# Kernel optimization log

Measured on AMD Instinct MI355X. Metric: run time of the kernel, lower is better.

## Reference

```python
import jax, jax.numpy as jnp
import numpy as np

EPS = 1e-5
N_HEADS = 16
D_NOPE = 128
D_ROPE = 64
D_QK = D_NOPE + D_ROPE  # 192
D_V = 128
KV_RANK = 512
SCALE = D_QK ** -0.5


def rms_norm(x, w, eps=EPS):
    return x * jax.lax.rsqrt(jnp.mean(x * x, axis=-1, keepdims=True) + eps) * w


def apply_rope(x, c, s):
    # x: [..., D_ROPE], c/s broadcastable [..., D_ROPE//2]; half-split rotation
    x0, x1 = x[..., : D_ROPE // 2], x[..., D_ROPE // 2 :]
    return jnp.concatenate([x0 * c - x1 * s, x0 * s + x1 * c], axis=-1)


def setup_inputs() -> dict:
    key = jax.random.key(0)
    ks = jax.random.split(key, 8)
    B, S, H_DIM = 2, 2048, 2048
    Q_RANK = 1536
    w = lambda k, shp: jax.random.normal(k, shp, dtype=jnp.float32) * 0.02
    # real RoPE tables: [max_seq, D_ROPE//2]
    inv_freq = 1.0 / (10000.0 ** (np.arange(0, D_ROPE, 2, dtype=np.float32) / D_ROPE))
    ang = np.arange(S, dtype=np.float32)[:, None] * inv_freq[None, :]
    return {
        "x": jax.random.normal(ks[0], (B, S, H_DIM), dtype=jnp.float32),
        "positions": jnp.arange(S, dtype=jnp.int64),
        "Wqa": w(ks[1], (H_DIM, Q_RANK)),
        "g_qa": jnp.ones((Q_RANK,), jnp.float32),
        "Wqb": w(ks[2], (Q_RANK, N_HEADS * D_QK)),
        "Wkva": w(ks[3], (H_DIM, KV_RANK + D_ROPE)),
        "g_kva": jnp.ones((KV_RANK,), jnp.float32),
        "Wkvb": w(ks[4], (KV_RANK, N_HEADS * (D_NOPE + D_V))),
        "Wo": w(ks[5], (N_HEADS * D_V, H_DIM)),
        "cos": jnp.asarray(np.cos(ang)),
        "sin": jnp.asarray(np.sin(ang)),
    }


def reference(x, positions, Wqa, g_qa, Wqb, Wkva, g_kva, Wkvb, Wo, cos, sin):
    B, S, _ = x.shape
    # Q path: low-rank down, RMSNorm, up
    q = rms_norm(x @ Wqa, g_qa) @ Wqb  # [B,S,H*D_QK]
    q = q.reshape(B, S, N_HEADS, D_QK)
    q_nope, q_rope = q[..., :D_NOPE], q[..., D_NOPE:]
    c = cos[positions]  # [S, D_ROPE//2]
    s = sin[positions]
    q_rope = apply_rope(q_rope, c[None, :, None, :], s[None, :, None, :])
    # KV path: joint down-proj, split latent / rope-key
    kv_a = x @ Wkva  # [B,S,KV_RANK+D_ROPE]
    kv_latent = rms_norm(kv_a[..., :KV_RANK], g_kva)
    k_rope = apply_rope(kv_a[..., KV_RANK:], c[None, :, :], s[None, :, :])  # [B,S,D_ROPE]
    # up-project latent to per-head k_nope and v
    kv_b = (kv_latent @ Wkvb).reshape(B, S, N_HEADS, D_NOPE + D_V)
    k_nope, v = kv_b[..., :D_NOPE], kv_b[..., D_NOPE:]
    k = jnp.concatenate(
        [k_nope, jnp.broadcast_to(k_rope[:, :, None, :], (B, S, N_HEADS, D_ROPE))], axis=-1
    )  # [B,S,H,D_QK]
    q_full = jnp.concatenate([q_nope, q_rope], axis=-1)  # [B,S,H,D_QK]
    # causal SDPA with d_qk != d_v
    scores = jnp.einsum("bqhd,bkhd->bhqk", q_full, k) * SCALE
    causal = jnp.tril(jnp.ones((S, S), dtype=bool))
    scores = jnp.where(causal[None, None, :, :], scores, -jnp.inf)
    p = jax.nn.softmax(scores, axis=-1)
    out = jnp.einsum("bhqk,bkhd->bqhd", p, v).reshape(B, S, N_HEADS * D_V)
    return out @ Wo
```

## Files before the change

kernel.cpp:

```cpp
#include <hip/hip_runtime.h>
#include <hip/hip_bf16.h>

typedef __bf16 bf16;
typedef __bf16 bf16x8 __attribute__((ext_vector_type(8)));
typedef __bf16 bf16x4 __attribute__((ext_vector_type(4)));
typedef float f32x4 __attribute__((ext_vector_type(4)));

#define B_    2
#define S_    2048
#define HD    2048
#define NH    16
#define DQK   192
#define DV    128
#define QR    1536
#define KVR   512
#define NTOK  4096
#define NKVB  4096
#define NQB   3072
#define NQKVA 2176

#define EXP2F(x) __builtin_amdgcn_exp2f(x)

static __device__ __forceinline__ void gload16(const void* g, void* l) {
  __builtin_amdgcn_global_load_lds(
      (const __attribute__((address_space(1))) void*)g,
      (__attribute__((address_space(3))) void*)l, 16, 0, 0);
}

__global__ __launch_bounds__(256) void cvt_bf16(const float* __restrict__ in,
                                                bf16* __restrict__ out, long n) {
  long i = ((long)blockIdx.x * 256 + threadIdx.x) * 4;
  if (i + 3 < n) {
    float4 v = *(const float4*)(in + i);
    bf16x4 o = {(bf16)v.x, (bf16)v.y, (bf16)v.z, (bf16)v.w};
    *(bf16x4*)(out + i) = o;
  }
}

struct TransArgs {
  const float *s0, *s1, *s2, *s3, *s4;
  bf16 *d0, *d1, *d2, *d3, *d4;
};
__global__ __launch_bounds__(256) void transpose_all(TransArgs a) {
  __shared__ float tile[32][33];
  int bid = blockIdx.x;
  int seg, rel;
  if      (bid < 3072)  { seg = 0; rel = bid; }
  else if (bid < 4352)  { seg = 1; rel = bid - 3072; }
  else if (bid < 8960)  { seg = 2; rel = bid - 4352; }
  else if (bid < 11008) { seg = 3; rel = bid - 8960; }
  else                  { seg = 4; rel = bid - 11008; }
  const float* in = seg == 0 ? a.s0 : seg == 1 ? a.s1 : seg == 2 ? a.s2 : seg == 3 ? a.s3 : a.s4;
  bf16* out       = seg == 0 ? a.d0 : seg == 1 ? a.d1 : seg == 2 ? a.d2 : seg == 3 ? a.d3 : a.d4;
  int R   = seg == 0 ? 2048 : seg == 1 ? 2048 : seg == 2 ? 1536 : seg == 3 ? 512 : 2048;
  int C   = seg == 0 ? 1536 : seg == 1 ? 576  : seg == 2 ? 3072 : seg == 3 ? 4096 : 2048;
  int Np  = seg == 0 ? 1536 : seg == 1 ? 640  : seg == 2 ? 3072 : seg == 3 ? 4096 : 2048;
  int nbx = seg == 0 ? 48   : seg == 1 ? 20   : seg == 2 ? 96   : seg == 3 ? 128 : 64;
  int c0 = (rel % nbx) * 32;
  int r0 = (rel / nbx) * 32;
  int tx = threadIdx.x & 31, ty = threadIdx.x >> 5;
#pragma unroll
  for (int i = 0; i < 4; ++i) {
    int r = r0 + ty + i * 8, c = c0 + tx;
    tile[ty + i * 8][tx] = (c < C) ? in[(long)r * C + c] : 0.f;
  }
  __syncthreads();
#pragma unroll
  for (int i = 0; i < 4; ++i) {
    int oc = c0 + ty + i * 8;
    if (oc < Np) out[(long)oc * R + r0 + tx] = (bf16)tile[tx][ty + i * 8];
  }
}

#define GEMM_CORE(A, Bt, K)                                                    \
  __shared__ bf16 As[128 * 64];                                                \
  __shared__ bf16 Bs[128 * 64];                                                \
  const int t = threadIdx.x;                                                   \
  const int l = t & 63;                                                        \
  const int w = t >> 6;                                                        \
  const int m0 = blockIdx.y * 128;                                             \
  const int n0 = blockIdx.x * 128;                                             \
  const int wr = (w >> 1) * 64;                                                \
  const int wc = (w & 1) * 64;                                                 \
  const int lr = l & 15;                                                       \
  const int lg = l >> 4;                                                       \
  f32x4 acc[4][4] = {};                                                        \
  for (int k0 = 0; k0 < (K); k0 += 64) {                                       \
    __syncthreads();                                                           \
    _Pragma("unroll")                                                          \
    for (int j = 0; j < 4; ++j) {                                              \
      int s = j * 256 + t;                                                     \
      int row = s >> 3, sc = s & 7;                                            \
      int c = sc ^ (row & 7);                                                  \
      gload16((A) + (long)(m0 + row) * (K) + k0 + c * 8,                       \
              As + (j * 256 + w * 64) * 8);                                    \
      gload16((Bt) + (long)(n0 + row) * (K) + k0 + c * 8,                      \
              Bs + (j * 256 + w * 64) * 8);                                    \
    }                                                                          \
    __syncthreads();                                                           \
    _Pragma("unroll")                                                          \
    for (int kh = 0; kh < 2; ++kh) {                                           \
      bf16x8 af[4], bfr[4];                                                    \
      _Pragma("unroll")                                                        \
      for (int m = 0; m < 4; ++m) {                                            \
        int row = wr + m * 16 + lr;                                            \
        af[m] = *(const bf16x8*)(As + row * 64 + (((kh * 4 + lg) ^ (row & 7)) << 3)); \
      }                                                                        \
      _Pragma("unroll")                                                        \
      for (int n = 0; n < 4; ++n) {                                            \
        int row = wc + n * 16 + lr;                                            \
        bfr[n] = *(const bf16x8*)(Bs + row * 64 + (((kh * 4 + lg) ^ (row & 7)) << 3)); \
      }                                                                        \
      _Pragma("unroll")                                                        \
      for (int m = 0; m < 4; ++m)                                              \
        _Pragma("unroll")                                                      \
        for (int n = 0; n < 4; ++n)                                            \
          acc[m][n] = __builtin_amdgcn_mfma_f32_16x16x32_bf16(af[m], bfr[n], acc[m][n], 0, 0, 0); \
    }                                                                          \
  }

template <typename CT>
__global__ __launch_bounds__(256) void gemm_bf16(const bf16* __restrict__ A,
                                                 const bf16* __restrict__ Bt,
                                                 CT* __restrict__ C,
                                                 int M, int N, int K) {
  GEMM_CORE(A, Bt, K)
#pragma unroll
  for (int m = 0; m < 4; ++m)
#pragma unroll
    for (int n = 0; n < 4; ++n)
#pragma unroll
      for (int v = 0; v < 4; ++v) {
        int row = m0 + wr + m * 16 + lg * 4 + v;
        int col = n0 + wc + n * 16 + lr;
        C[(long)row * N + col] = (CT)acc[m][n][v];
      }
}

__global__ __launch_bounds__(256) void gemm_qf(const bf16* __restrict__ A,
                                               const bf16* __restrict__ Bt,
                                               const int* __restrict__ pos,
                                               const float* __restrict__ cosT,
                                               const float* __restrict__ sinT,
                                               bf16* __restrict__ q_bhsd) {
  const float SCALE = 0.07216878364870323f * 1.4426950408889634f;
  GEMM_CORE(A, Bt, QR)
  int c0 = n0 + wc;
  int h = c0 / 192;
  int part = c0 - h * 192;
#pragma unroll
  for (int m = 0; m < 4; ++m)
#pragma unroll
    for (int v = 0; v < 4; ++v) {
      int row = m0 + wr + m * 16 + lg * 4 + v;
      int b = row >> 11, s = row & (S_ - 1);
      long base = ((long)(b * NH + h) * S_ + s) * DQK;
      if (part < 128) {
#pragma unroll
        for (int n = 0; n < 4; ++n)
          q_bhsd[base + part + n * 16 + lr] = (bf16)(acc[m][n][v] * SCALE);
      } else {
        int p = pos[s] & (S_ - 1);
        float c_lo = cosT[p * 32 + lr],      s_lo = sinT[p * 32 + lr];
        float c_hi = cosT[p * 32 + 16 + lr], s_hi = sinT[p * 32 + 16 + lr];
        float o0 = acc[m][0][v] * c_lo - acc[m][2][v] * s_lo;
        float o1 = acc[m][1][v] * c_hi - acc[m][3][v] * s_hi;
        float o2 = acc[m][0][v] * s_lo + acc[m][2][v] * c_lo;
        float o3 = acc[m][1][v] * s_hi + acc[m][3][v] * c_hi;
        q_bhsd[base + 128 + lr] = (bf16)(o0 * SCALE);
        q_bhsd[base + 144 + lr] = (bf16)(o1 * SCALE);
        q_bhsd[base + 160 + lr] = (bf16)(o2 * SCALE);
        q_bhsd[base + 176 + lr] = (bf16)(o3 * SCALE);
      }
    }
}

__global__ __launch_bounds__(256) void gemm_kvb(const bf16* __restrict__ A,
                                                const bf16* __restrict__ Bt,
                                                bf16* __restrict__ k_bhsd,
                                                bf16* __restrict__ v_rows) {
  GEMM_CORE(A, Bt, KVR)
  int c0 = n0 + wc;
  int h = c0 >> 8;
  int dbase = c0 & 64;
  bool vpart = (c0 >> 7) & 1;
#pragma unroll
  for (int m = 0; m < 4; ++m)
#pragma unroll
    for (int v = 0; v < 4; ++v) {
      int row = m0 + wr + m * 16 + lg * 4 + v;
      int b = row >> 11, s = row & (S_ - 1);
      if (!vpart) {
        long base = ((long)(b * NH + h) * S_ + s) * DQK + dbase;
#pragma unroll
        for (int n = 0; n < 4; ++n)
          k_bhsd[base + n * 16 + lr] = (bf16)acc[m][n][v];
      } else {
        long base = (long)row * 2048 + h * 128 + dbase;
#pragma unroll
        for (int n = 0; n < 4; ++n)
          v_rows[base + n * 16 + lr] = (bf16)acc[m][n][v];
      }
    }
}

__global__ __launch_bounds__(256) void norm_prep(const bf16* __restrict__ xa,
                                                 const float* __restrict__ g_qa,
                                                 const float* __restrict__ g_kva,
                                                 const int* __restrict__ pos,
                                                 const float* __restrict__ cosT,
                                                 const float* __restrict__ sinT,
                                                 bf16* __restrict__ q_n,
                                                 bf16* __restrict__ kv_l,
                                                 bf16* __restrict__ k_bhsd) {
  int row = blockIdx.x;
  int t = threadIdx.x;
  int b = row >> 11, s = row & (S_ - 1);
  const bf16* xr = xa + (long)row * NQKVA;
  __shared__ float red[3];
  __shared__ bf16 rope_s[64];
  float vf[8];
  if (t < 192) {
    bf16x8 vv = *(const bf16x8*)(xr + t * 8);
    float ss = 0.f;
#pragma unroll
    for (int e = 0; e < 8; ++e) { vf[e] = (float)vv[e]; ss += vf[e] * vf[e]; }
#pragma unroll
    for (int m = 1; m < 64; m <<= 1) ss += __shfl_xor(ss, m);
    if ((t & 63) == 0) red[t >> 6] = ss;
  } else {
    int tt = t - 192;
    const bf16* xl = xr + QR;
    bf16x8 vv = *(const bf16x8*)(xl + tt * 8);
    float ss = 0.f;
#pragma unroll
    for (int e = 0; e < 8; ++e) { vf[e] = (float)vv[e]; ss += vf[e] * vf[e]; }
#pragma unroll
    for (int m = 1; m < 64; m <<= 1) ss += __shfl_xor(ss, m);
    float rs = rsqrtf(ss / KVR + 1e-5f);
    bf16x8 o;
#pragma unroll
    for (int e = 0; e < 8; ++e) o[e] = (bf16)(vf[e] * rs * g_kva[tt * 8 + e]);
    *(bf16x8*)(kv_l + (long)row * KVR + tt * 8) = o;
    if (tt < 32) {
      int p = pos[s] & (S_ - 1);
      float c = cosT[p * 32 + tt], sn = sinT[p * 32 + tt];
      float x0 = (float)xl[512 + tt], x1 = (float)xl[544 + tt];
      rope_s[tt] = (bf16)(x0 * c - x1 * sn);
      rope_s[32 + tt] = (bf16)(x0 * sn + x1 * c);
    }
  }
  __syncthreads();
  if (t < 192) {
    float ss = red[0] + red[1] + red[2];
    float rs = rsqrtf(ss / QR + 1e-5f);
    bf16x8 o;
#pragma unroll
    for (int e = 0; e < 8; ++e) o[e] = (bf16)(vf[e] * rs * g_qa[t * 8 + e]);
    *(bf16x8*)(q_n + (long)row * QR + t * 8) = o;
  } else {
    int tt = t - 192;
    bf16x8 rv = *(const bf16x8*)&rope_s[(tt & 7) * 8];
    long base0 = ((long)(b * NH + (tt >> 3)) * S_ + s) * DQK + 128 + (tt & 7) * 8;
    long base1 = ((long)(b * NH + 8 + (tt >> 3)) * S_ + s) * DQK + 128 + (tt & 7) * 8;
    *(bf16x8*)(k_bhsd + base0) = rv;
    *(bf16x8*)(k_bhsd + base1) = rv;
  }
}

__global__ __launch_bounds__(256) void v_trans(const bf16* __restrict__ v_rows,
                                               bf16* __restrict__ v_t) {
  __shared__ bf16 tile[32][33];
  int st = blockIdx.x, dt = blockIdx.y, bh = blockIdx.z;
  int b = bh >> 4, h = bh & 15;
  int tx = threadIdx.x & 31, ty = threadIdx.x >> 5;
#pragma unroll
  for (int i = 0; i < 4; ++i) {
    int s = st * 32 + ty + i * 8, d = dt * 32 + tx;
    tile[ty + i * 8][tx] = v_rows[((long)(b * S_ + s)) * 2048 + h * 128 + d];
  }
  __syncthreads();
#pragma unroll
  for (int i = 0; i < 4; ++i) {
    int d = dt * 32 + ty + i * 8, s = st * 32 + tx;
    v_t[((long)bh * DV + d) * S_ + s] = tile[tx][ty + i * 8];
  }
}

#define QBLK 64
#define KVB  64
#define DVP  144
__global__ __launch_bounds__(256) void flash2(const bf16* __restrict__ q_bhsd,
                                              const bf16* __restrict__ k_bhsd,
                                              const bf16* __restrict__ v_t,
                                              bf16* __restrict__ att) {
  __shared__ bf16 Ks[KVB * DQK];
  __shared__ bf16 Vs[DVP * KVB];
  __shared__ bf16 Ps[4][16 * 72];
  int bid = blockIdx.x;
  int bh = bid & 31;
  int qt = 31 - (bid >> 5);
  int b = bh >> 4, h = bh & 15;
  int q0 = qt * QBLK;
  int t = threadIdx.x;
  int w = t >> 6, l = t & 63;
  int lr = l & 15, lg = l >> 4;
  int qw = q0 + w * 16;

  const bf16* Qb = q_bhsd + (long)bh * S_ * DQK;
  const bf16* Kb = k_bhsd + (long)bh * S_ * DQK;
  const bf16* Vb = v_t + (long)bh * DV * S_;

  if (t < 128) {
    int rr = 128 + (t >> 3), cc = (t & 7) * 8;
    bf16 val = (bf16)((rr == 128) ? 1.0f : 0.0f);
    bf16x8 vvv = {val, val, val, val, val, val, val, val};
    *(bf16x8*)(Vs + rr * KVB + cc) = vvv;
  }

  bf16x8 qf[6];
#pragma unroll
  for (int t6 = 0; t6 < 6; ++t6)
    qf[t6] = *(const bf16x8*)(Qb + (long)(qw + lr) * DQK + t6 * 32 + lg * 8);

  f32x4 oacc[9] = {};
  float mrow[4] = {-1e30f, -1e30f, -1e30f, -1e30f};
  const int lr7 = lr & 7;

  int nkt = qt + 1;
  for (int kt = 0; kt < nkt; ++kt) {
    int k0 = kt * KVB;
    __syncthreads();
#pragma unroll
    for (int j = 0; j < 6; ++j) {
      int s = j * 256 + t;
      int r = s / 24, c1 = s - r * 24;
      int c = c1 ^ (r & 7);
      gload16(Kb + (long)(k0 + r) * DQK + c * 8, Ks + (j * 256 + w * 64) * 8);
    }
#pragma unroll
    for (int j = 0; j < 4; ++j) {
      int s = j * 256 + t;
      int d = s >> 3, c1 = s & 7;
      int c = c1 ^ (d & 7);
      gload16(Vb + (long)d * S_ + k0 + c * 8, Vs + (j * 256 + w * 64) * 8);
    }
    __syncthreads();
    if (k0 > qw + 15) continue;

    f32x4 sacc[4] = {};
#pragma unroll
    for (int n = 0; n < 4; ++n) {
      int rk = n * 16 + lr;
#pragma unroll
      for (int t6 = 0; t6 < 6; ++t6) {
        bf16x8 kf = *(const bf16x8*)(Ks + rk * DQK + (((t6 * 4 + lg) ^ lr7) << 3));
        sacc[n] = __builtin_amdgcn_mfma_f32_16x16x32_bf16(qf[t6], kf, sacc[n], 0, 0, 0);
      }
    }
    if (k0 + KVB - 1 > qw) {
#pragma unroll
      for (int n = 0; n < 4; ++n)
#pragma unroll
        for (int v = 0; v < 4; ++v) {
          int r = lg * 4 + v, c = n * 16 + lr;
          if (k0 + c > qw + r) sacc[n][v] = -1e30f;
        }
    }
    float mv[4];
#pragma unroll
    for (int v = 0; v < 4; ++v) {
      mv[v] = fmaxf(fmaxf(sacc[0][v], sacc[1][v]), fmaxf(sacc[2][v], sacc[3][v]));
#pragma unroll
      for (int msk = 1; msk < 16; msk <<= 1) mv[v] = fmaxf(mv[v], __shfl_xor(mv[v], msk));
    }
    bool grow = (mv[0] > mrow[0] + 8.f) | (mv[1] > mrow[1] + 8.f) |
                (mv[2] > mrow[2] + 8.f) | (mv[3] > mrow[3] + 8.f);
    if (__any(grow)) {
      float corr[4];
#pragma unroll
      for (int v = 0; v < 4; ++v) {
        float mt = fmaxf(mrow[v], mv[v]);
        corr[v] = EXP2F(mrow[v] - mt);
        mrow[v] = mt;
      }
#pragma unroll
      for (int dn = 0; dn < 9; ++dn)
#pragma unroll
        for (int v = 0; v < 4; ++v) oacc[dn][v] *= corr[v];
    }
#pragma unroll
    for (int v = 0; v < 4; ++v)
#pragma unroll
      for (int n = 0; n < 4; ++n)
        Ps[w][(lg * 4 + v) * 72 + n * 16 + lr] = (bf16)EXP2F(sacc[n][v] - mrow[v]);
#pragma unroll
    for (int kc = 0; kc < 2; ++kc) {
      bf16x8 pf = *(const bf16x8*)(Ps[w] + lr * 72 + kc * 32 + lg * 8);
#pragma unroll
      for (int dn = 0; dn < 9; ++dn) {
        int d = dn * 16 + lr;
        bf16x8 vf = *(const bf16x8*)(Vs + d * KVB + (((kc * 4 + lg) ^ lr7) << 3));
        oacc[dn] = __builtin_amdgcn_mfma_f32_16x16x32_bf16(pf, vf, oacc[dn], 0, 0, 0);
      }
    }
  }
  float rl[4];
#pragma unroll
  for (int v = 0; v < 4; ++v) {
    float lv = __shfl(oacc[8][v], lg * 16);
    rl[v] = 1.0f / lv;
  }
#pragma unroll
  for (int dn = 0; dn < 8; ++dn)
#pragma unroll
    for (int v = 0; v < 4; ++v) {
      int r = lg * 4 + v;
      float o = oacc[dn][v] * rl[v];
      att[((long)(b * S_ + qw + r)) * 2048 + h * 128 + dn * 16 + lr] = (bf16)o;
    }
}

extern "C" void kernel_launch(void* const* d_in, const int* in_sizes, int n_in,
                              void* d_out, int out_size, void* d_ws, size_t ws_size,
                              hipStream_t stream) {
  const float* x        = (const float*)d_in[0];
  const int* pos        = (const int*)d_in[1];
  const float* Wqa      = (const float*)d_in[2];
  const float* g_qa     = (const float*)d_in[3];
  const float* Wqb      = (const float*)d_in[4];
  const float* Wkva     = (const float*)d_in[5];
  const float* g_kva    = (const float*)d_in[6];
  const float* Wkvb     = (const float*)d_in[7];
  const float* Wo       = (const float*)d_in[8];
  const float* cosT     = (const float*)d_in[9];
  const float* sinT     = (const float*)d_in[10];
  float* out            = (float*)d_out;

  size_t off = 0;
  char* wsp = (char*)d_ws;
  auto alloc = [&](size_t n) { void* p = wsp + off; off += (n + 255) & ~(size_t)255; return p; };
  bf16*  Wqa_t  = (bf16*) alloc((size_t)QR * HD * 2);
  bf16*  Wkva_t = (bf16*) alloc((size_t)640 * HD * 2);
  bf16*  Wqb_t  = (bf16*) alloc((size_t)NQB * QR * 2);
  bf16*  Wkvb_t = (bf16*) alloc((size_t)NKVB * KVR * 2);
  bf16*  Wo_t   = (bf16*) alloc((size_t)HD * HD * 2);
  bf16*  x_bf   = (bf16*) alloc((size_t)NTOK * HD * 2);
  bf16*  q_bhsd = (bf16*) alloc((size_t)B_ * NH * S_ * DQK * 2);
  bf16*  k_bhsd = (bf16*) alloc((size_t)B_ * NH * S_ * DQK * 2);
  bf16*  v_rows = (bf16*) alloc((size_t)NTOK * 2048 * 2);
  bf16*  v_t    = (bf16*) alloc((size_t)B_ * NH * DV * S_ * 2);
  bf16*  att    = (bf16*) alloc((size_t)NTOK * 2048 * 2);
  char*  T      = (char*) alloc((size_t)33554432);
  bf16*  xa  = (bf16*)T;
  bf16*  q_n = (bf16*)(T + 18874368);
  bf16*  kv_l = (bf16*)(T + 18874368 + 12582912);
  if (ws_size < off) return;

  cvt_bf16<<<(NTOK * HD / 4 + 255) / 256, 256, 0, stream>>>(x, x_bf, (long)NTOK * HD);
  TransArgs ta = {Wqa, Wkva, Wqb, Wkvb, Wo, Wqa_t, Wkva_t, Wqb_t, Wkvb_t, Wo_t};
  transpose_all<<<15104, 256, 0, stream>>>(ta);
  gemm_bf16<bf16><<<dim3(NQKVA / 128, NTOK / 128), 256, 0, stream>>>(x_bf, Wqa_t, xa, NTOK, NQKVA, HD);
  norm_prep<<<NTOK, 256, 0, stream>>>(xa, g_qa, g_kva, pos, cosT, sinT, q_n, kv_l, k_bhsd);
  gemm_qf<<<dim3(NQB / 128, NTOK / 128), 256, 0, stream>>>(q_n, Wqb_t, pos, cosT, sinT, q_bhsd);
  gemm_kvb<<<dim3(NKVB / 128, NTOK / 128), 256, 0, stream>>>(kv_l, Wkvb_t, k_bhsd, v_rows);
  v_trans<<<dim3(S_ / 32, DV / 32, B_ * NH), 256, 0, stream>>>(v_rows, v_t);
  flash2<<<1024, 256, 0, stream>>>(q_bhsd, k_bhsd, v_t, att);
  gemm_bf16<float><<<dim3(HD / 128, NTOK / 128), 256, 0, stream>>>(att, Wo_t, out, NTOK, HD, HD);
}
```

Baseline: 325.3 us.

## Fuse V transpose into KV-up GEMM epilogue and enlarge flash query tile

The KV up-projection epilogue now writes V directly in transposed [b,h,d,s] layout as 4-wide bf16 stores, so the separate v_trans kernel and the v_rows buffer are removed. The attention kernel is widened to 512 threads (8 waves) with 128-query tiles, which halves the number of blocks and shares each K/V tile load across twice as many query rows. The trade-offs are narrower strided stores in the GEMM epilogue, more causal-tail imbalance per block, and higher shared-memory and register pressure per block.

```diff
diff --git a/kernel.cpp b/kernel.cpp
--- a/kernel.cpp
+++ b/kernel.cpp
@@ -178,30 +178,38 @@
 __global__ __launch_bounds__(256) void gemm_kvb(const bf16* __restrict__ A,
                                                 const bf16* __restrict__ Bt,
                                                 bf16* __restrict__ k_bhsd,
-                                                bf16* __restrict__ v_rows) {
+                                                bf16* __restrict__ v_t) {
   GEMM_CORE(A, Bt, KVR)
   int c0 = n0 + wc;
   int h = c0 >> 8;
   int dbase = c0 & 64;
   bool vpart = (c0 >> 7) & 1;
-#pragma unroll
-  for (int m = 0; m < 4; ++m)
-#pragma unroll
-    for (int v = 0; v < 4; ++v) {
-      int row = m0 + wr + m * 16 + lg * 4 + v;
-      int b = row >> 11, s = row & (S_ - 1);
-      if (!vpart) {
+  if (!vpart) {
+#pragma unroll
+    for (int m = 0; m < 4; ++m)
+#pragma unroll
+      for (int v = 0; v < 4; ++v) {
+        int row = m0 + wr + m * 16 + lg * 4 + v;
+        int b = row >> 11, s = row & (S_ - 1);
         long base = ((long)(b * NH + h) * S_ + s) * DQK + dbase;
 #pragma unroll
         for (int n = 0; n < 4; ++n)
           k_bhsd[base + n * 16 + lr] = (bf16)acc[m][n][v];
-      } else {
-        long base = (long)row * 2048 + h * 128 + dbase;
-#pragma unroll
-        for (int n = 0; n < 4; ++n)
-          v_rows[base + n * 16 + lr] = (bf16)acc[m][n][v];
-      }
-    }
+      }
+  } else {
+#pragma unroll
+    for (int m = 0; m < 4; ++m) {
+      int row0 = m0 + wr + m * 16 + lg * 4;
+      int b = row0 >> 11, s = row0 & (S_ - 1);
+#pragma unroll
+      for (int n = 0; n < 4; ++n) {
+        int d = dbase + n * 16 + lr;
+        bf16x4 o = {(bf16)acc[m][n][0], (bf16)acc[m][n][1],
+                    (bf16)acc[m][n][2], (bf16)acc[m][n][3]};
+        *(bf16x4*)(v_t + ((long)(b * NH + h) * DV + d) * S_ + s) = o;
+      }
+    }
+  }
 }
 
 __global__ __launch_bounds__(256) void norm_prep(const bf16* __restrict__ xa,
@@ -268,40 +276,20 @@
   }
 }
 
-__global__ __launch_bounds__(256) void v_trans(const bf16* __restrict__ v_rows,
-                                               bf16* __restrict__ v_t) {
-  __shared__ bf16 tile[32][33];
-  int st = blockIdx.x, dt = blockIdx.y, bh = blockIdx.z;
-  int b = bh >> 4, h = bh & 15;
-  int tx = threadIdx.x & 31, ty = threadIdx.x >> 5;
-#pragma unroll
-  for (int i = 0; i < 4; ++i) {
-    int s = st * 32 + ty + i * 8, d = dt * 32 + tx;
-    tile[ty + i * 8][tx] = v_rows[((long)(b * S_ + s)) * 2048 + h * 128 + d];
-  }
-  __syncthreads();
-#pragma unroll
-  for (int i = 0; i < 4; ++i) {
-    int d = dt * 32 + ty + i * 8, s = st * 32 + tx;
-    v_t[((long)bh * DV + d) * S_ + s] = tile[tx][ty + i * 8];
-  }
-}
-
-#define QBLK 64
 #define KVB  64
 #define DVP  144
-__global__ __launch_bounds__(256) void flash2(const bf16* __restrict__ q_bhsd,
+__global__ __launch_bounds__(512) void flash4(const bf16* __restrict__ q_bhsd,
                                               const bf16* __restrict__ k_bhsd,
                                               const bf16* __restrict__ v_t,
                                               bf16* __restrict__ att) {
   __shared__ bf16 Ks[KVB * DQK];
   __shared__ bf16 Vs[DVP * KVB];
-  __shared__ bf16 Ps[4][16 * 72];
+  __shared__ bf16 Ps[8][16 * 72];
   int bid = blockIdx.x;
   int bh = bid & 31;
-  int qt = 31 - (bid >> 5);
+  int qt = 15 - (bid >> 5);
   int b = bh >> 4, h = bh & 15;
-  int q0 = qt * QBLK;
+  int q0 = qt * 128;
   int t = threadIdx.x;
   int w = t >> 6, l = t & 63;
   int lr = l & 15, lg = l >> 4;
@@ -327,23 +315,23 @@
   float mrow[4] = {-1e30f, -1e30f, -1e30f, -1e30f};
   const int lr7 = lr & 7;
 
-  int nkt = qt + 1;
+  int nkt = 2 * qt + 2;
   for (int kt = 0; kt < nkt; ++kt) {
     int k0 = kt * KVB;
     __syncthreads();
 #pragma unroll
-    for (int j = 0; j < 6; ++j) {
-      int s = j * 256 + t;
+    for (int j = 0; j < 3; ++j) {
+      int s = j * 512 + t;
       int r = s / 24, c1 = s - r * 24;
       int c = c1 ^ (r & 7);
-      gload16(Kb + (long)(k0 + r) * DQK + c * 8, Ks + (j * 256 + w * 64) * 8);
-    }
-#pragma unroll
-    for (int j = 0; j < 4; ++j) {
-      int s = j * 256 + t;
+      gload16(Kb + (long)(k0 + r) * DQK + c * 8, Ks + (j * 512 + w * 64) * 8);
+    }
+#pragma unroll
+    for (int j = 0; j < 2; ++j) {
+      int s = j * 512 + t;
       int d = s >> 3, c1 = s & 7;
       int c = c1 ^ (d & 7);
-      gload16(Vb + (long)d * S_ + k0 + c * 8, Vs + (j * 256 + w * 64) * 8);
+      gload16(Vb + (long)d * S_ + k0 + c * 8, Vs + (j * 512 + w * 64) * 8);
     }
     __syncthreads();
     if (k0 > qw + 15) continue;
@@ -448,7 +436,6 @@
   bf16*  x_bf   = (bf16*) alloc((size_t)NTOK * HD * 2);
   bf16*  q_bhsd = (bf16*) alloc((size_t)B_ * NH * S_ * DQK * 2);
   bf16*  k_bhsd = (bf16*) alloc((size_t)B_ * NH * S_ * DQK * 2);
-  bf16*  v_rows = (bf16*) alloc((size_t)NTOK * 2048 * 2);
   bf16*  v_t    = (bf16*) alloc((size_t)B_ * NH * DV * S_ * 2);
   bf16*  att    = (bf16*) alloc((size_t)NTOK * 2048 * 2);
   char*  T      = (char*) alloc((size_t)33554432);
@@ -463,8 +450,7 @@
   gemm_bf16<bf16><<<dim3(NQKVA / 128, NTOK / 128), 256, 0, stream>>>(x_bf, Wqa_t, xa, NTOK, NQKVA, HD);
   norm_prep<<<NTOK, 256, 0, stream>>>(xa, g_qa, g_kva, pos, cosT, sinT, q_n, kv_l, k_bhsd);
   gemm_qf<<<dim3(NQB / 128, NTOK / 128), 256, 0, stream>>>(q_n, Wqb_t, pos, cosT, sinT, q_bhsd);
-  gemm_kvb<<<dim3(NKVB / 128, NTOK / 128), 256, 0, stream>>>(kv_l, Wkvb_t, k_bhsd, v_rows);
-  v_trans<<<dim3(S_ / 32, DV / 32, B_ * NH), 256, 0, stream>>>(v_rows, v_t);
-  flash2<<<1024, 256, 0, stream>>>(q_bhsd, k_bhsd, v_t, att);
+  gemm_kvb<<<dim3(NKVB / 128, NTOK / 128), 256, 0, stream>>>(kv_l, Wkvb_t, k_bhsd, v_t);
+  flash4<<<512, 512, 0, stream>>>(q_bhsd, k_bhsd, v_t, att);
   gemm_bf16<float><<<dim3(HD / 128, NTOK / 128), 256, 0, stream>>>(att, Wo_t, out, NTOK, HD, HD);
 }
```

Measured after the change: 320.1 us. No clear change (-1.6%).
